# Optimization experiments

Hardware: AMD Instinct MI355X
Metric: run time of the kernel (lower is better)

## Reference

```python
import jax, jax.numpy as jnp
import numpy as np
import math

TOPK = 32

def setup_inputs() -> dict:
    key = jax.random.key(0)
    k1, k2, k3, k4 = jax.random.split(key, 4)
    B, D_e, D_o, T, H, W = 2, 128, 256, 16, 64, 64
    H_ref = W_ref = 32  # resolution_ref = 2
    THW_ref = T * H_ref * W_ref
    HW_ref = H_ref * W_ref
    return {
        "m_in": jax.random.normal(k1, (B, D_e, T, H, W), jnp.float32),
        "m_out": jax.random.normal(k2, (B, D_o, T, H, W), jnp.float32),
        "q_in": jax.random.normal(k3, (B, D_e, H, W), jnp.float32),
        "qk_ref": jax.random.normal(k4, (B, THW_ref, HW_ref), jnp.float32),
    }


def reference(m_in, m_out, q_in, qk_ref):
    B, D_e, T, H, W = m_in.shape
    D_o = m_out.shape[1]
    _, THW_ref, HW_ref = qk_ref.shape
    res = int(math.sqrt(H * W // HW_ref))
    H_ref, W_ref = H // res, W // res
    s = res
    k = TOPK

    # top-k memory blocks for each of the HW_ref query blocks
    topk_val, topk_idx = jax.lax.top_k(jnp.swapaxes(qk_ref, 1, 2), k)  # [B, HW_ref, k]
    # torch path scatters one-hot then uses nonzero -> gather order is ascending-index;
    # softmax-attention over n is permutation invariant, but sort for exact faithfulness.
    idx_sorted = jnp.sort(topk_idx, axis=-1)

    def blockify(m, D):
        # [B,D,T,H,W] -> [B, T*H_ref*W_ref, s, s, D]
        m = m.reshape(B, D, T, H_ref, s, W_ref, s)
        m = m.transpose(0, 2, 3, 5, 4, 6, 1)  # B,T,H_ref,W_ref,s,s,D
        return m.reshape(B, T * H_ref * W_ref, s, s, D)

    m_in_b = blockify(m_in, D_e)
    m_out_b = blockify(m_out, D_o)

    flat_idx = idx_sorted.reshape(B, HW_ref * k)
    gather = jax.vmap(lambda mb, i: mb[i])  # per-batch fancy gather of blocks
    m_in_sel = gather(m_in_b, flat_idx).reshape(B, H_ref, W_ref, k * s * s, D_e)
    m_out_sel = gather(m_out_b, flat_idx).reshape(B, H_ref, W_ref, k * s * s, D_o)

    # query blocks: [B, H_ref, W_ref, D_e, s, s]
    q = q_in.reshape(B, D_e, H_ref, s, W_ref, s).transpose(0, 2, 4, 1, 3, 5)

    p = jnp.einsum('bhwnc,bhwcij->bhwijn', m_in_sel, q) / math.sqrt(D_e)
    p = jax.nn.softmax(p, axis=-1)
    mem_out = jnp.einsum('bhwnc,bhwijn->bchiwj', m_out_sel, p).reshape(B, D_o, H, W)

    kk = max(k // 4, 1)
    return mem_out, topk_idx[:, :, :kk], topk_val[:, :, :kk]
```

## Files before the change

### kernel.cpp

```cpp
#include <hip/hip_runtime.h>
#include <math.h>



__device__ inline unsigned mono_u32(float f) {
    unsigned b = __float_as_uint(f);
    return (b & 0x80000000u) ? ~b : (b | 0x80000000u);
}

__global__ __launch_bounds__(256) void qk_chunk_max(const float* __restrict__ qk,
                                                    float* __restrict__ Mx) {
    int wg = blockIdx.x;
    int chunk = wg & 511;
    int b = wg >> 9;
    int tid = threadIdx.x;
    const float4* p = (const float4*)(qk + ((size_t)b * 16384 + (size_t)chunk * 32) * 1024) + tid;
    float4 m4;
    m4.x = m4.y = m4.z = m4.w = -__builtin_inff();
#pragma unroll
    for (int rb = 0; rb < 4; ++rb) {
        float4 v[8];
#pragma unroll
        for (int u = 0; u < 8; ++u)
            v[u] = p[(size_t)(rb * 8 + u) * 256];
#pragma unroll
        for (int u = 0; u < 8; ++u) {
            m4.x = fmaxf(m4.x, v[u].x); m4.y = fmaxf(m4.y, v[u].y);
            m4.z = fmaxf(m4.z, v[u].z); m4.w = fmaxf(m4.w, v[u].w);
        }
    }
    ((float4*)Mx)[(size_t)wg * 256 + tid] = m4;
}

__global__ __launch_bounds__(256) void qk_thresh(const float* __restrict__ Mx,
                                                 unsigned* __restrict__ t_u,
                                                 int* __restrict__ cnt) {
    int colg = blockIdx.x;
    int tid = threadIdx.x;
    int b = colg >> 10, col = colg & 1023;
    const float* base = Mx + (size_t)b * 524288 + col;
    unsigned u0 = mono_u32(base[(size_t)tid * 1024]);
    unsigned u1 = mono_u32(base[(size_t)(tid + 256) * 1024]);

    __shared__ int hist1[256];
    __shared__ int hist2[256];
    __shared__ int s_b1, s_above1;
    __shared__ unsigned s_tu;
    hist1[tid] = 0; hist2[tid] = 0;
    __syncthreads();

    atomicAdd(&hist1[u0 >> 24], 1);
    atomicAdd(&hist1[u1 >> 24], 1);
    __syncthreads();

    if (tid < 64) {
        int base4 = 252 - 4 * tid;
        int h0 = hist1[base4], h1 = hist1[base4 + 1], h2 = hist1[base4 + 2], h3 = hist1[base4 + 3];
        int gs = h0 + h1 + h2 + h3;
        int pre = gs;
#pragma unroll
        for (int off = 1; off < 64; off <<= 1) {
            int o = __shfl_up(pre, off, 64);
            if (tid >= off) pre += o;
        }
        int excl = pre - gs;
        if (excl < 32 && pre >= 32) {
            int c = excl, bb, ab;
            c += h3; if (c >= 32) { bb = base4 + 3; ab = c - h3; }
            else { c += h2; if (c >= 32) { bb = base4 + 2; ab = c - h2; }
            else { c += h1; if (c >= 32) { bb = base4 + 1; ab = c - h1; }
            else { c += h0;   bb = base4;     ab = c - h0; } } }
            s_b1 = bb; s_above1 = ab;
        }
    }
    __syncthreads();
    int b1 = s_b1;
    if ((int)(u0 >> 24) == b1) atomicAdd(&hist2[(u0 >> 16) & 0xFF], 1);
    if ((int)(u1 >> 24) == b1) atomicAdd(&hist2[(u1 >> 16) & 0xFF], 1);
    __syncthreads();

    if (tid < 64) {
        int A = s_above1;
        int base4 = 252 - 4 * tid;
        int h0 = hist2[base4], h1 = hist2[base4 + 1], h2 = hist2[base4 + 2], h3 = hist2[base4 + 3];
        int gs = h0 + h1 + h2 + h3;
        int pre = gs;
#pragma unroll
        for (int off = 1; off < 64; off <<= 1) {
            int o = __shfl_up(pre, off, 64);
            if (tid >= off) pre += o;
        }
        int excl = pre - gs;
        if (A + excl < 32 && A + pre >= 32) {
            int c = A + excl, bb;
            c += h3; if (c >= 32) bb = base4 + 3;
            else { c += h2; if (c >= 32) bb = base4 + 2;
            else { c += h1; if (c >= 32) bb = base4 + 1;
            else { bb = base4; } } }
            s_tu = (((unsigned)b1 << 8) | (unsigned)bb) << 16;
        }
    }
    __syncthreads();
    if (tid == 0) { t_u[colg] = s_tu; cnt[colg] = 0; }
}

__global__ __launch_bounds__(256) void qk_filter(const float* __restrict__ qk,
                                                 const unsigned* __restrict__ t_u,
                                                 int* __restrict__ cnt,
                                                 unsigned long long* __restrict__ cand) {
    int wg = blockIdx.x;
    int chunk = wg & 511;
    int b = wg >> 9;
    int tid = threadIdx.x;
    const float4* p = (const float4*)(qk + ((size_t)b * 16384 + (size_t)chunk * 32) * 1024) + tid;
    uint4 tu = ((const uint4*)t_u)[b * 256 + tid];

    unsigned mxm = 0, mym = 0, mzm = 0, mwm = 0;
#pragma unroll
    for (int rb = 0; rb < 4; ++rb) {
        float4 v[8];
#pragma unroll
        for (int u = 0; u < 8; ++u)
            v[u] = p[(size_t)(rb * 8 + u) * 256];
#pragma unroll
        for (int u = 0; u < 8; ++u) {
            int r = rb * 8 + u;
            mxm |= (mono_u32(v[u].x) >= tu.x ? 1u : 0u) << r;
            mym |= (mono_u32(v[u].y) >= tu.y ? 1u : 0u) << r;
            mzm |= (mono_u32(v[u].z) >= tu.z ? 1u : 0u) << r;
            mwm |= (mono_u32(v[u].w) >= tu.w ? 1u : 0u) << r;
        }
    }

    int row0 = chunk * 32;
    int colg0 = b * 1024 + 4 * tid;
    const float* q0 = qk + ((size_t)b * 16384 + row0) * 1024 + 4 * tid;
    unsigned msk[4] = {mxm, mym, mzm, mwm};
#pragma unroll
    for (int j = 0; j < 4; ++j) {
        unsigned m = msk[j];
        while (m) {
            int r = __ffs(m) - 1;
            m &= m - 1;
            unsigned uu = mono_u32(q0[(size_t)r * 1024 + j]);
            int pos = atomicAdd(&cnt[colg0 + j], 1);
            if (pos < 256)
                cand[(size_t)(colg0 + j) * 256 + pos] =
                    ((unsigned long long)uu << 32) |
                    (unsigned long long)(16383 - (row0 + r));
        }
    }
}

__global__ __launch_bounds__(256) void topk_select(const unsigned long long* __restrict__ cand,
                                                   const int* __restrict__ cnt,
                                                   const float* __restrict__ qk,
                                                   float* __restrict__ out_idx,
                                                   float* __restrict__ out_val,
                                                   int* __restrict__ idx_sorted) {
    int bid = blockIdx.x;
    int tid = threadIdx.x;
    __shared__ unsigned long long sc[256];
    __shared__ unsigned long long selk[32];

    int C = cnt[bid];
    if (C <= 256) {
        if (tid < C) sc[tid] = cand[(size_t)bid * 256 + tid];
        __syncthreads();
        if (tid < C) {
            unsigned long long mine = sc[tid];
            int rank = 0;
            for (int j = 0; j < C; ++j) rank += (sc[j] > mine) ? 1 : 0;
            if (rank < 32) selk[rank] = mine;
        }
        __syncthreads();
    } else {
        int b = bid >> 10, q = bid & 1023;
        const float* colp = qk + (size_t)b * 16384 * 1024 + q;
        unsigned long long prev = ~0ull;
#pragma unroll 1
        for (int s = 0; s < 32; ++s) {
            unsigned long long best = 0;
            for (int r = tid; r < 16384; r += 256) {
                unsigned long long k =
                    ((unsigned long long)mono_u32(colp[(size_t)r * 1024]) << 32) |
                    (unsigned long long)(16383 - r);
                if (k < prev && k > best) best = k;
            }
            sc[tid] = best;
            __syncthreads();
            for (int off = 128; off >= 1; off >>= 1) {
                if (tid < off && sc[tid + off] > sc[tid]) sc[tid] = sc[tid + off];
                __syncthreads();
            }
            if (tid == 0) selk[s] = sc[0];
            __syncthreads();
            prev = selk[s];
        }
    }

    if (tid < 8) {
        unsigned long long k = selk[tid];
        unsigned uv = (unsigned)(k >> 32);
        unsigned bits = (uv & 0x80000000u) ? (uv ^ 0x80000000u) : ~uv;
        out_val[(size_t)bid * 8 + tid] = __uint_as_float(bits);
        int gi = 16383 - (int)(k & 0xFFFFFFFFull);
        out_idx[(size_t)bid * 8 + tid] = (float)gi;
    }
    if (tid < 32) {
        int mine = 16383 - (int)(selk[tid] & 0xFFFFFFFFull);
        int rank = 0;
#pragma unroll
        for (int j = 0; j < 32; ++j) {
            int oj = 16383 - (int)(selk[j] & 0xFFFFFFFFull);
            rank += (oj < mine) ? 1 : 0;
        }
        idx_sorted[(size_t)bid * 32 + rank] = mine;
    }
}

template <int D, int T>
__global__ __launch_bounds__(256) void blockify2(const float* __restrict__ in,
                                                 float* __restrict__ out) {
    constexpr int NH = D / 128;
    __shared__ float tile[128][128];
    int wg = blockIdx.x;
    int h  = wg % NH;
    int hb = (wg / NH) % 32;
    int t  = (wg / (NH * 32)) % T;
    int b  = wg / (NH * 32 * T);
    int tid = threadIdx.x;

    {
        int m   = tid & 31;
        int cl0 = tid >> 5;
        float4 v[16];
#pragma unroll
        for (int pass = 0; pass < 16; ++pass) {
            int c = pass * 8 + cl0;
            const float* src = in +
                ((size_t)(b * D + h * 128 + c) * T + t) * 4096 + (size_t)hb * 128;
            v[pass] = *(const float4*)(src + 4 * m);
        }
#pragma unroll
        for (int pass = 0; pass < 16; ++pass) {
            int c = pass * 8 + cl0;
            int sw = ((c >> 2) & 31) << 2;
            *(float4*)&tile[c][(4 * m) ^ sw] = v[pass];
        }
    }
    __syncthreads();

    {
        size_t slab = (((size_t)b * T + t) * 1024 + (size_t)hb * 32) * (4 * D) +
                      (size_t)h * 128;
#pragma unroll
        for (int it = 0; it < 16; ++it) {
            int flat = it * 1024 + tid * 4;
            int cl = flat & 127;
            int pp = (flat >> 7) & 3;
            int wb = flat >> 9;
            int pos = ((pp >> 1) << 6) + 2 * wb + (pp & 1);
            int sw = ((cl >> 2) & 31) << 2;
            float4 o;
            o.x = tile[cl + 0][pos ^ sw];
            o.y = tile[cl + 1][pos ^ sw];
            o.z = tile[cl + 2][pos ^ sw];
            o.w = tile[cl + 3][pos ^ sw];
            *(float4*)(out + slab + (size_t)wb * 4 * D + (size_t)pp * D + cl) = o;
        }
    }
}

__global__ __launch_bounds__(256) void attn_kernel(const float* __restrict__ m_in_b,
                                                   const float* __restrict__ m_out_b,
                                                   const float* __restrict__ q_b,
                                                   const int* __restrict__ idx_sorted,
                                                   float* __restrict__ out) {
    int bid = blockIdx.x;
    int b = bid >> 10, qblk = bid & 1023;
    int hb = qblk >> 5, wb = qblk & 31;
    int tid = threadIdx.x;
    int w = tid >> 6, lane = tid & 63;

    __shared__ float K[64][129];
    __shared__ float Q[4][128];
    __shared__ float P[4][128];
    __shared__ int   blks[32];

    if (tid < 32) blks[tid] = idx_sorted[(size_t)bid * 32 + tid];
    {
        const float* qsrc = q_b + (size_t)bid * 512;
        ((float*)Q)[tid]       = qsrc[tid];
        ((float*)Q)[tid + 256] = qsrc[tid + 256];
    }
    __syncthreads();

    const float scale = 0.08838834764831845f;
    float s01[2];
#pragma unroll 1
    for (int half = 0; half < 2; ++half) {
        if (half) __syncthreads();
#pragma unroll 4
        for (int ki = 0; ki < 16; ++ki) {
            int blk = blks[half * 16 + ki];
            const float* src = m_in_b + ((size_t)b * 16384 + blk) * 512;
            int p0 = tid >> 7, c0 = tid & 127;
            K[ki * 4 + p0][c0]     = src[tid];
            K[ki * 4 + p0 + 2][c0] = src[tid + 256];
        }
        __syncthreads();
        float acc = 0.f;
#pragma unroll 4
        for (int c = 0; c < 128; ++c) acc += K[lane][c] * Q[w][c];
        s01[half] = acc * scale;
    }

    float m = fmaxf(s01[0], s01[1]);
#pragma unroll
    for (int off = 32; off >= 1; off >>= 1) m = fmaxf(m, __shfl_xor(m, off, 64));
    float e0 = expf(s01[0] - m), e1 = expf(s01[1] - m);
    float sum = e0 + e1;
#pragma unroll
    for (int off = 32; off >= 1; off >>= 1) sum += __shfl_xor(sum, off, 64);
    float inv = 1.0f / sum;
    P[w][lane]      = e0 * inv;
    P[w][lane + 64] = e1 * inv;
    __syncthreads();

    float a0 = 0.f, a1 = 0.f, a2 = 0.f, a3 = 0.f;
    int d = tid;
#pragma unroll 1
    for (int ki = 0; ki < 32; ++ki) {
        const float* vsrc = m_out_b + ((size_t)b * 16384 + blks[ki]) * 1024;
#pragma unroll
        for (int p = 0; p < 4; ++p) {
            float vv = vsrc[p * 256 + d];
            int n = ki * 4 + p;
            a0 += P[0][n] * vv; a1 += P[1][n] * vv;
            a2 += P[2][n] * vv; a3 += P[3][n] * vv;
        }
    }
    size_t base = (((size_t)b * 256 + d) * 64 + hb * 2) * 64 + wb * 2;
    out[base]      = a0;
    out[base + 1]  = a1;
    out[base + 64] = a2;
    out[base + 65] = a3;
}

extern "C" void kernel_launch(void* const* d_in, const int* in_sizes, int n_in,
                              void* d_out, int out_size, void* d_ws, size_t ws_size,
                              hipStream_t stream) {
    const float* m_in  = (const float*)d_in[0];
    const float* m_out = (const float*)d_in[1];
    const float* q_in  = (const float*)d_in[2];
    const float* qk    = (const float*)d_in[3];

    char* ws = (char*)d_ws;
    float* m_out_b = (float*)(ws);
    float* m_in_b  = (float*)(ws + 134217728);
    float* q_b     = (float*)(ws + 201326592);
    int*   idxs    = (int*)  (ws + 205520896);

    unsigned long long* cand = (unsigned long long*)(ws);
    float*    Mx  = (float*)   (ws + 4194304);
    unsigned* t_u = (unsigned*)(ws + 8388608);
    int*      cnt = (int*)     (ws + 8396800);

    float* out     = (float*)d_out;
    float* out_mem = out;
    float* out_idx = out + 2097152;
    float* out_val = out + 2113536;

    qk_chunk_max<<<1024, 256, 0, stream>>>(qk, Mx);
    qk_thresh   <<<2048, 256, 0, stream>>>(Mx, t_u, cnt);
    qk_filter   <<<1024, 256, 0, stream>>>(qk, t_u, cnt, cand);
    topk_select <<<2048, 256, 0, stream>>>(cand, cnt, qk, out_idx, out_val, idxs);

    blockify2<128, 16><<<1024, 256, 0, stream>>>(m_in, m_in_b);
    blockify2<128, 1><<<64, 256, 0, stream>>>(q_in, q_b);
    blockify2<256, 16><<<2048, 256, 0, stream>>>(m_out, m_out_b);
    attn_kernel<<<2048, 256, 0, stream>>>(m_in_b, m_out_b, q_b, idxs, out_mem);
}
```

Measured before the change: 472.2 us.

## Vectorize attention kernel loads and split PV accumulation across waves

The K tile load into shared memory now uses float4 global reads and an XOR-swizzled LDS layout, and the QK dot product reads float4s from LDS. The PV stage is restructured so each wave handles a quarter of the 32 memory blocks, with each lane owning four channels loaded as float4. The per-wave partial sums are then reduced through shared memory and written as float2 pairs. The aim is fewer, wider memory transactions and more independent loads in flight, at the cost of extra registers and one more barrier.

```diff
diff --git a/kernel.cpp b/kernel.cpp
--- a/kernel.cpp
+++ b/kernel.cpp
@@ -272,6 +272,8 @@
     }
 }
 
+__device__ inline int kidx(int r, int g) { return r * 128 + (((g ^ (r & 7))) << 2); }
+
 __global__ __launch_bounds__(256) void attn_kernel(const float* __restrict__ m_in_b,
                                                    const float* __restrict__ m_out_b,
                                                    const float* __restrict__ q_b,
@@ -283,16 +285,15 @@
     int tid = threadIdx.x;
     int w = tid >> 6, lane = tid & 63;
 
-    __shared__ float K[64][129];
-    __shared__ float Q[4][128];
-    __shared__ float P[4][128];
-    __shared__ int   blks[32];
+    __shared__ __align__(16) float Kbuf[64 * 128];
+    __shared__ __align__(16) float Q[4][128];
+    __shared__ __align__(16) float P[4][128];
+    __shared__ int blks[32];
 
     if (tid < 32) blks[tid] = idx_sorted[(size_t)bid * 32 + tid];
-    {
-        const float* qsrc = q_b + (size_t)bid * 512;
-        ((float*)Q)[tid]       = qsrc[tid];
-        ((float*)Q)[tid + 256] = qsrc[tid + 256];
+    if (tid < 128) {
+        float4 qv = ((const float4*)(q_b + (size_t)bid * 512))[tid];
+        *(float4*)((float*)Q + tid * 4) = qv;
     }
     __syncthreads();
 
@@ -301,18 +302,25 @@
 #pragma unroll 1
     for (int half = 0; half < 2; ++half) {
         if (half) __syncthreads();
-#pragma unroll 4
-        for (int ki = 0; ki < 16; ++ki) {
-            int blk = blks[half * 16 + ki];
-            const float* src = m_in_b + ((size_t)b * 16384 + blk) * 512;
-            int p0 = tid >> 7, c0 = tid & 127;
-            K[ki * 4 + p0][c0]     = src[tid];
-            K[ki * 4 + p0 + 2][c0] = src[tid + 256];
+#pragma unroll
+        for (int it = 0; it < 8; ++it) {
+            int flat = it * 256 + tid;
+            int ki = flat >> 7, l = flat & 127;
+            const float4* src = (const float4*)(m_in_b +
+                ((size_t)b * 16384 + blks[half * 16 + ki]) * 512);
+            float4 v = src[l];
+            int r = ki * 4 + (l >> 5);
+            int g = l & 31;
+            *(float4*)&Kbuf[kidx(r, g)] = v;
         }
         __syncthreads();
         float acc = 0.f;
-#pragma unroll 4
-        for (int c = 0; c < 128; ++c) acc += K[lane][c] * Q[w][c];
+#pragma unroll
+        for (int c4 = 0; c4 < 32; ++c4) {
+            float4 k4 = *(const float4*)&Kbuf[kidx(lane, c4)];
+            float4 q4 = *(const float4*)&Q[w][c4 << 2];
+            acc += k4.x * q4.x + k4.y * q4.y + k4.z * q4.z + k4.w * q4.w;
+        }
         s01[half] = acc * scale;
     }
 
@@ -328,24 +336,59 @@
     P[w][lane + 64] = e1 * inv;
     __syncthreads();
 
-    float a0 = 0.f, a1 = 0.f, a2 = 0.f, a3 = 0.f;
-    int d = tid;
-#pragma unroll 1
-    for (int ki = 0; ki < 32; ++ki) {
-        const float* vsrc = m_out_b + ((size_t)b * 16384 + blks[ki]) * 1024;
-#pragma unroll
-        for (int p = 0; p < 4; ++p) {
-            float vv = vsrc[p * 256 + d];
-            int n = ki * 4 + p;
-            a0 += P[0][n] * vv; a1 += P[1][n] * vv;
-            a2 += P[2][n] * vv; a3 += P[3][n] * vv;
-        }
-    }
-    size_t base = (((size_t)b * 256 + d) * 64 + hb * 2) * 64 + wb * 2;
-    out[base]      = a0;
-    out[base + 1]  = a1;
-    out[base + 64] = a2;
-    out[base + 65] = a3;
+    float a[16];
+#pragma unroll
+    for (int i = 0; i < 16; ++i) a[i] = 0.f;
+    int c4b = lane << 2;
+#pragma unroll
+    for (int nq = 0; nq < 8; ++nq) {
+        int n0 = (w << 5) + (nq << 2);
+        float4 p0 = *(const float4*)&P[0][n0];
+        float4 p1 = *(const float4*)&P[1][n0];
+        float4 p2 = *(const float4*)&P[2][n0];
+        float4 p3 = *(const float4*)&P[3][n0];
+        const float* vbase = m_out_b +
+            ((size_t)b * 16384 + blks[(w << 3) + nq]) * 1024 + c4b;
+        float4 v0 = *(const float4*)(vbase);
+        float4 v1 = *(const float4*)(vbase + 256);
+        float4 v2 = *(const float4*)(vbase + 512);
+        float4 v3 = *(const float4*)(vbase + 768);
+#define ACC4(vj, px, py, pz, pw)                                          \
+        a[0]  += px * vj.x; a[1]  += py * vj.x; a[2]  += pz * vj.x; a[3]  += pw * vj.x; \
+        a[4]  += px * vj.y; a[5]  += py * vj.y; a[6]  += pz * vj.y; a[7]  += pw * vj.y; \
+        a[8]  += px * vj.z; a[9]  += py * vj.z; a[10] += pz * vj.z; a[11] += pw * vj.z; \
+        a[12] += px * vj.w; a[13] += py * vj.w; a[14] += pz * vj.w; a[15] += pw * vj.w;
+        ACC4(v0, p0.x, p1.x, p2.x, p3.x)
+        ACC4(v1, p0.y, p1.y, p2.y, p3.y)
+        ACC4(v2, p0.z, p1.z, p2.z, p3.z)
+        ACC4(v3, p0.w, p1.w, p2.w, p3.w)
+#undef ACC4
+    }
+
+    float* red = Kbuf;
+    {
+        int rb = (w * 64 + lane) * 16;
+        *(float4*)&red[rb + 0]  = make_float4(a[0],  a[1],  a[2],  a[3]);
+        *(float4*)&red[rb + 4]  = make_float4(a[4],  a[5],  a[6],  a[7]);
+        *(float4*)&red[rb + 8]  = make_float4(a[8],  a[9],  a[10], a[11]);
+        *(float4*)&red[rb + 12] = make_float4(a[12], a[13], a[14], a[15]);
+    }
+    __syncthreads();
+    {
+        int ch = tid;
+        int off = (ch >> 2) * 16 + (ch & 3) * 4;
+        float4 r0 = *(const float4*)&red[0 * 1024 + off];
+        float4 r1 = *(const float4*)&red[1 * 1024 + off];
+        float4 r2 = *(const float4*)&red[2 * 1024 + off];
+        float4 r3 = *(const float4*)&red[3 * 1024 + off];
+        float o0 = r0.x + r1.x + r2.x + r3.x;
+        float o1 = r0.y + r1.y + r2.y + r3.y;
+        float o2 = r0.z + r1.z + r2.z + r3.z;
+        float o3 = r0.w + r1.w + r2.w + r3.w;
+        size_t base = (((size_t)b * 256 + ch) * 64 + hb * 2) * 64 + wb * 2;
+        *(float2*)&out[base]      = make_float2(o0, o1);
+        *(float2*)&out[base + 64] = make_float2(o2, o3);
+    }
 }
 
 extern "C" void kernel_launch(void* const* d_in, const int* in_sizes, int n_in,
```

New measurement: 468.7 us. Within noise of the previous version (-0.7%).
